# Performance work log

Hardware: AMD Instinct MI355X
Metric: run time of the kernel (lower is better)

## Reference

```python
import jax, jax.numpy as jnp
import numpy as np

N = 50000   # nodes
E = 800000  # edges (avg degree 16)
D = 128     # in = hidden = out channels (residual path active)
EPS = 1e-5  # BatchNorm eps


def setup_inputs() -> dict:
    key = jax.random.key(0)
    ks = jax.random.split(key, 24)
    sc = 1.0 / np.sqrt(D)
    inp = {
        "x": jax.random.normal(ks[0], (N, D), jnp.float32),
        "W1": jax.random.normal(ks[1], (D, D), jnp.float32) * sc,
        "b1": jnp.zeros((D,), jnp.float32),
        "g1": 1.0 + 0.1 * jax.random.normal(ks[2], (D,), jnp.float32),
        "be1": 0.1 * jax.random.normal(ks[3], (D,), jnp.float32),
        "m1": 0.1 * jax.random.normal(ks[4], (D,), jnp.float32),
        "v1": 0.5 + jax.random.uniform(ks[5], (D,), jnp.float32),
        "W2": jax.random.normal(ks[6], (D, D), jnp.float32) * sc,
        "b2": jnp.zeros((D,), jnp.float32),
        "g2": 1.0 + 0.1 * jax.random.normal(ks[7], (D,), jnp.float32),
        "be2": 0.1 * jax.random.normal(ks[8], (D,), jnp.float32),
        "m2": 0.1 * jax.random.normal(ks[9], (D,), jnp.float32),
        "v2": 0.5 + jax.random.uniform(ks[10], (D,), jnp.float32),
        "W3": jax.random.normal(ks[11], (D, D), jnp.float32) * sc,
        "b3": jnp.zeros((D,), jnp.float32),
        "src": jax.random.randint(ks[12], (E,), 0, N, jnp.int32),
        "dst": jax.random.randint(ks[13], (E,), 0, N, jnp.int32),
    }
    return inp


def _gcn_conv(x, W, b, src, dst):
    # PyG GCNConv: add self-loops, symmetric D^{-1/2}(A+I)D^{-1/2} normalization.
    h = x @ W                                              # [N, C]
    deg = jax.ops.segment_sum(jnp.ones((E,), x.dtype), dst, num_segments=N) + 1.0
    dinv = jax.lax.rsqrt(deg)                              # [N]
    coef = dinv[src] * dinv[dst]                           # [E]
    agg = jax.ops.segment_sum(h[src] * coef[:, None], dst, num_segments=N)
    agg = agg + h * (dinv * dinv)[:, None]                 # self-loop term
    return agg + b


def _bn(x, g, be, m, v):
    # eval-mode BatchNorm1d with running stats
    return (x - m) * jax.lax.rsqrt(v + EPS) * g + be


def reference(x, W1, b1, g1, be1, m1, v1, W2, b2, g2, be2, m2, v2, W3, b3, src, dst):
    x_res = x
    h = jax.nn.relu(_bn(_gcn_conv(x, W1, b1, src, dst), g1, be1, m1, v1))
    h = jax.nn.relu(_bn(_gcn_conv(h, W2, b2, src, dst), g2, be2, m2, v2))
    h = _gcn_conv(h, W3, b3, src, dst)
    return h + x_res  # in_channels == out_channels -> residual active
```

## Files before the change

### kernel.cpp

```cpp
#include <hip/hip_runtime.h>
#include <hip/hip_bf16.h>


#define GCN_N 50000
#define GCN_E 800000
#define GCN_D 128

using bf16x8 = __attribute__((ext_vector_type(8))) short;
using f32x4  = __attribute__((ext_vector_type(4))) float;

__device__ __forceinline__ float bflo(unsigned u) { return __uint_as_float(u << 16); }
__device__ __forceinline__ float bfhi(unsigned u) { return __uint_as_float(u & 0xffff0000u); }
__device__ __forceinline__ unsigned f2bf(float f) {
    unsigned u = __float_as_uint(f);
    return (u + 0x7fffu + ((u >> 16) & 1u)) >> 16;
}

__global__ __launch_bounds__(256) void zero_kernel(int* __restrict__ p, int n) {
    int i = blockIdx.x * blockDim.x + threadIdx.x;
    if (i < n) p[i] = 0;
}

__global__ __launch_bounds__(256) void hist_kernel(const int* __restrict__ dst,
                                                   int* __restrict__ cnt, int nE) {
    int e = blockIdx.x * blockDim.x + threadIdx.x;
    if (e < nE) atomicAdd(&cnt[dst[e]], 1);
}

__global__ __launch_bounds__(256) void block_reduce(const int* __restrict__ cnt,
                                                    int* __restrict__ bsum, int n) {
    int tid = threadIdx.x, lane = tid & 63, wid = tid >> 6;
    int i0 = blockIdx.x * 1024 + tid * 4;
    int s = 0;
    #pragma unroll
    for (int q = 0; q < 4; ++q)
        if (i0 + q < n) s += cnt[i0 + q];
    #pragma unroll
    for (int off = 32; off >= 1; off >>= 1) s += __shfl_xor(s, off);
    __shared__ int ws[4];
    if (lane == 0) ws[wid] = s;
    __syncthreads();
    if (tid == 0) bsum[blockIdx.x] = ws[0] + ws[1] + ws[2] + ws[3];
}

__global__ void scan_bsums(const int* __restrict__ bsum, int* __restrict__ boff,
                           int nb, int* __restrict__ row_last) {
    int lane = threadIdx.x;
    int v = (lane < nb) ? bsum[lane] : 0;
    int sc = v;
    #pragma unroll
    for (int off = 1; off < 64; off <<= 1) {
        int t = __shfl_up(sc, off);
        if (lane >= off) sc += t;
    }
    if (lane < nb) boff[lane] = sc - v;
    if (lane == 63) *row_last = sc;
}

__global__ __launch_bounds__(256) void scan_apply(const int* __restrict__ cnt_in,
                                                  const int* __restrict__ boff,
                                                  int* __restrict__ row_ptr,
                                                  float* __restrict__ dinv,
                                                  int* __restrict__ cnt_zero, int n) {
    __shared__ int wsum[4];
    int tid = threadIdx.x, lane = tid & 63, wid = tid >> 6;
    int i0 = blockIdx.x * 1024 + tid * 4;
    int a0 = 0, a1 = 0, a2 = 0, a3 = 0;
    if (i0 + 0 < n) a0 = cnt_in[i0 + 0];
    if (i0 + 1 < n) a1 = cnt_in[i0 + 1];
    if (i0 + 2 < n) a2 = cnt_in[i0 + 2];
    if (i0 + 3 < n) a3 = cnt_in[i0 + 3];
    int tsum = a0 + a1 + a2 + a3;
    int sc = tsum;
    #pragma unroll
    for (int off = 1; off < 64; off <<= 1) {
        int t = __shfl_up(sc, off);
        if (lane >= off) sc += t;
    }
    if (lane == 63) wsum[wid] = sc;
    __syncthreads();
    int woff = 0;
    #pragma unroll
    for (int w = 0; w < 4; ++w)
        if (w < wid) woff += wsum[w];
    int excl = boff[blockIdx.x] + woff + (sc - tsum);
    if (i0 + 0 < n) { row_ptr[i0 + 0] = excl;                dinv[i0 + 0] = rsqrtf((float)a0 + 1.f); cnt_zero[i0 + 0] = 0; }
    if (i0 + 1 < n) { row_ptr[i0 + 1] = excl + a0;           dinv[i0 + 1] = rsqrtf((float)a1 + 1.f); cnt_zero[i0 + 1] = 0; }
    if (i0 + 2 < n) { row_ptr[i0 + 2] = excl + a0 + a1;      dinv[i0 + 2] = rsqrtf((float)a2 + 1.f); cnt_zero[i0 + 2] = 0; }
    if (i0 + 3 < n) { row_ptr[i0 + 3] = excl + a0 + a1 + a2; dinv[i0 + 3] = rsqrtf((float)a3 + 1.f); cnt_zero[i0 + 3] = 0; }
}

__global__ __launch_bounds__(256) void fill_kernel(const int* __restrict__ src,
                                                   const int* __restrict__ dst,
                                                   const int* __restrict__ row_ptr,
                                                   int* __restrict__ cur,
                                                   int* __restrict__ esrc, int nE) {
    int e = blockIdx.x * blockDim.x + threadIdx.x;
    if (e >= nE) return;
    int d = dst[e];
    int pos = row_ptr[d] + atomicAdd(&cur[d], 1);
    esrc[pos] = src[e];
}

__global__ void prep_kernel(const float* __restrict__ b, const float* __restrict__ g,
                            const float* __restrict__ be, const float* __restrict__ m,
                            const float* __restrict__ v, float* __restrict__ scale,
                            float* __restrict__ shift) {
    int c = threadIdx.x;
    float s = g[c] * rsqrtf(v[c] + 1e-5f);
    scale[c] = s;
    shift[c] = (b[c] - m[c]) * s + be[c];
}

__global__ __launch_bounds__(256) void castx_kernel(const float* __restrict__ x,
                                                    unsigned short* __restrict__ xb,
                                                    int nElem) {
    int i = (blockIdx.x * 256 + threadIdx.x) * 8;
    if (i + 7 < nElem) {
        float4 f0 = *(const float4*)&x[i];
        float4 f1 = *(const float4*)&x[i + 4];
        uint4 o;
        o.x = f2bf(f0.x) | (f2bf(f0.y) << 16);
        o.y = f2bf(f0.z) | (f2bf(f0.w) << 16);
        o.z = f2bf(f1.x) | (f2bf(f1.y) << 16);
        o.w = f2bf(f1.z) | (f2bf(f1.w) << 16);
        *(uint4*)&xb[i] = o;
    }
}

__global__ __launch_bounds__(256) void wtrans_kernel(const float* __restrict__ W,
                                                     unsigned short* __restrict__ Wt) {
    int id = blockIdx.x * 256 + threadIdx.x;
    int nn = id >> 7, k = id & 127;
    Wt[id] = (unsigned short)f2bf(W[k * 128 + nn]);
}

__global__ __launch_bounds__(256) void mm_mfma(const unsigned short* __restrict__ A,
                                               const unsigned short* __restrict__ Wt,
                                               const float* __restrict__ dinv,
                                               unsigned short* __restrict__ hb, int n) {
    __shared__ unsigned short Cs[64][136];
    int tid = threadIdx.x;
    int w = tid >> 6, l = tid & 63;
    int lg = l >> 4, li = l & 15;
    int row0 = blockIdx.x * 64;

    int arow = row0 + w * 16 + li;
    int arow_c = min(arow, n - 1);
    const unsigned short* ap = A + (size_t)arow_c * GCN_D + lg * 8;
    bf16x8 a[4];
    #pragma unroll
    for (int k0 = 0; k0 < 4; ++k0) a[k0] = *(const bf16x8*)(ap + k0 * 32);

    f32x4 acc[8];
    #pragma unroll
    for (int t = 0; t < 8; ++t) acc[t] = (f32x4){0.f, 0.f, 0.f, 0.f};

    #pragma unroll
    for (int t = 0; t < 8; ++t) {
        const unsigned short* bp = Wt + (size_t)(t * 16 + li) * GCN_D + lg * 8;
        #pragma unroll
        for (int k0 = 0; k0 < 4; ++k0) {
            bf16x8 b = *(const bf16x8*)(bp + k0 * 32);
            acc[t] = __builtin_amdgcn_mfma_f32_16x16x32_bf16(a[k0], b, acc[t], 0, 0, 0);
        }
    }

    int crow = w * 16 + lg * 4;
    float dv[4];
    #pragma unroll
    for (int r = 0; r < 4; ++r) dv[r] = dinv[min(row0 + crow + r, n - 1)];
    #pragma unroll
    for (int t = 0; t < 8; ++t)
        #pragma unroll
        for (int r = 0; r < 4; ++r)
            Cs[crow + r][t * 16 + li] = (unsigned short)f2bf(acc[t][r] * dv[r]);
    __syncthreads();

    int orow = tid >> 2;
    int gr = row0 + orow;
    if (gr < n) {
        const unsigned short* sp = &Cs[orow][(tid & 3) * 32];
        uint4* dp = (uint4*)&hb[(size_t)gr * GCN_D + (tid & 3) * 32];
        dp[0] = *(const uint4*)(sp + 0);
        dp[1] = *(const uint4*)(sp + 8);
        dp[2] = *(const uint4*)(sp + 16);
        dp[3] = *(const uint4*)(sp + 24);
    }
}

template <int FINAL>
__global__ __launch_bounds__(256) void agg_kernel(const unsigned short* __restrict__ hb,
                                                  const int* __restrict__ row_ptr,
                                                  const int* __restrict__ esrc,
                                                  const float* __restrict__ dinv,
                                                  const float* __restrict__ scale,
                                                  const float* __restrict__ shift,
                                                  const float* __restrict__ xres,
                                                  unsigned short* __restrict__ outb,
                                                  float* __restrict__ outf, int n) {
    int wid = threadIdx.x >> 6, lane = threadIdx.x & 63;
    int node = blockIdx.x * 4 + wid;
    if (node >= n) return;
    int cc = lane * 2;
    unsigned us = *(const unsigned*)&hb[(size_t)node * GCN_D + cc];
    float aLo = bflo(us), aHi = bfhi(us);
    float bLo = 0.f, bHi = 0.f;
    int j = row_ptr[node], end = row_ptr[node + 1];
    for (; j + 8 <= end; j += 8) {
        int s0 = esrc[j + 0], s1 = esrc[j + 1], s2 = esrc[j + 2], s3 = esrc[j + 3];
        int s4 = esrc[j + 4], s5 = esrc[j + 5], s6 = esrc[j + 6], s7 = esrc[j + 7];
        unsigned u0 = *(const unsigned*)&hb[(size_t)s0 * GCN_D + cc];
        unsigned u1 = *(const unsigned*)&hb[(size_t)s1 * GCN_D + cc];
        unsigned u2 = *(const unsigned*)&hb[(size_t)s2 * GCN_D + cc];
        unsigned u3 = *(const unsigned*)&hb[(size_t)s3 * GCN_D + cc];
        unsigned u4 = *(const unsigned*)&hb[(size_t)s4 * GCN_D + cc];
        unsigned u5 = *(const unsigned*)&hb[(size_t)s5 * GCN_D + cc];
        unsigned u6 = *(const unsigned*)&hb[(size_t)s6 * GCN_D + cc];
        unsigned u7 = *(const unsigned*)&hb[(size_t)s7 * GCN_D + cc];
        aLo += bflo(u0) + bflo(u1);  aHi += bfhi(u0) + bfhi(u1);
        bLo += bflo(u2) + bflo(u3);  bHi += bfhi(u2) + bfhi(u3);
        aLo += bflo(u4) + bflo(u5);  aHi += bfhi(u4) + bfhi(u5);
        bLo += bflo(u6) + bflo(u7);  bHi += bfhi(u6) + bfhi(u7);
    }
    for (; j < end; ++j) {
        int s = esrc[j];
        unsigned u = *(const unsigned*)&hb[(size_t)s * GCN_D + cc];
        aLo += bflo(u);  aHi += bfhi(u);
    }
    float dvn = dinv[node];
    float vx = (aLo + bLo) * dvn;
    float vy = (aHi + bHi) * dvn;
    if (FINAL) {
        float2 b = *(const float2*)&scale[cc];
        float2 xr = *(const float2*)&xres[(size_t)node * GCN_D + cc];
        float2 o;
        o.x = vx + b.x + xr.x;
        o.y = vy + b.y + xr.y;
        *(float2*)&outf[(size_t)node * GCN_D + cc] = o;
    } else {
        float2 sc = *(const float2*)&scale[cc];
        float2 sh = *(const float2*)&shift[cc];
        float ox = fmaxf(vx * sc.x + sh.x, 0.f);
        float oy = fmaxf(vy * sc.y + sh.y, 0.f);
        *(unsigned*)&outb[(size_t)node * GCN_D + cc] = f2bf(ox) | (f2bf(oy) << 16);
    }
}

extern "C" void kernel_launch(void* const* d_in, const int* in_sizes, int n_in,
                              void* d_out, int out_size, void* d_ws, size_t ws_size,
                              hipStream_t stream) {
    (void)in_sizes; (void)n_in; (void)out_size; (void)ws_size;
    const int N = GCN_N, E = GCN_E, D = GCN_D;

    const float* x   = (const float*)d_in[0];
    const float* W1  = (const float*)d_in[1];
    const float* b1  = (const float*)d_in[2];
    const float* g1  = (const float*)d_in[3];
    const float* be1 = (const float*)d_in[4];
    const float* m1  = (const float*)d_in[5];
    const float* v1  = (const float*)d_in[6];
    const float* W2  = (const float*)d_in[7];
    const float* b2  = (const float*)d_in[8];
    const float* g2  = (const float*)d_in[9];
    const float* be2 = (const float*)d_in[10];
    const float* m2  = (const float*)d_in[11];
    const float* v2  = (const float*)d_in[12];
    const float* W3  = (const float*)d_in[13];
    const float* b3  = (const float*)d_in[14];
    const int* src   = (const int*)d_in[15];
    const int* dst   = (const int*)d_in[16];
    float* out = (float*)d_out;

    unsigned short* hb   = (unsigned short*)d_ws;
    unsigned short* actb = hb + (size_t)N * D;
    unsigned short* xb   = actb + (size_t)N * D;
    unsigned short* wt1  = xb + (size_t)N * D;
    unsigned short* wt2  = wt1 + D * D;
    unsigned short* wt3  = wt2 + D * D;
    float* dinv   = (float*)(wt3 + D * D);
    int* cnt      = (int*)(dinv + N);
    int* row_ptr  = cnt + N;
    int* esrc     = row_ptr + (N + 2);
    float* scale1 = (float*)(esrc + E);
    float* shift1 = scale1 + D;
    float* scale2 = shift1 + D;
    float* shift2 = scale2 + D;
    int* bsum     = (int*)(shift2 + D);
    int* boff     = bsum + 64;

    const int NB = (N + 1023) / 1024;

    castx_kernel<<<(N * D) / (256 * 8), 256, 0, stream>>>(x, xb, N * D);
    wtrans_kernel<<<(D * D) / 256, 256, 0, stream>>>(W1, wt1);
    wtrans_kernel<<<(D * D) / 256, 256, 0, stream>>>(W2, wt2);
    wtrans_kernel<<<(D * D) / 256, 256, 0, stream>>>(W3, wt3);
    zero_kernel<<<(N + 255) / 256, 256, 0, stream>>>(cnt, N);
    hist_kernel<<<(E + 255) / 256, 256, 0, stream>>>(dst, cnt, E);
    block_reduce<<<NB, 256, 0, stream>>>(cnt, bsum, N);
    scan_bsums<<<1, 64, 0, stream>>>(bsum, boff, NB, &row_ptr[N]);
    scan_apply<<<NB, 256, 0, stream>>>(cnt, boff, row_ptr, dinv, cnt, N);
    fill_kernel<<<(E + 255) / 256, 256, 0, stream>>>(src, dst, row_ptr, cnt, esrc, E);
    prep_kernel<<<1, D, 0, stream>>>(b1, g1, be1, m1, v1, scale1, shift1);
    prep_kernel<<<1, D, 0, stream>>>(b2, g2, be2, m2, v2, scale2, shift2);

    int mm_grid = (N + 63) / 64;
    int agg_grid = (N + 3) / 4;

    mm_mfma<<<mm_grid, 256, 0, stream>>>(xb, wt1, dinv, hb, N);
    agg_kernel<0><<<agg_grid, 256, 0, stream>>>(hb, row_ptr, esrc, dinv,
                                                scale1, shift1, nullptr, actb, nullptr, N);
    mm_mfma<<<mm_grid, 256, 0, stream>>>(actb, wt2, dinv, hb, N);
    agg_kernel<0><<<agg_grid, 256, 0, stream>>>(hb, row_ptr, esrc, dinv,
                                                scale2, shift2, nullptr, actb, nullptr, N);
    mm_mfma<<<mm_grid, 256, 0, stream>>>(actb, wt3, dinv, hb, N);
    agg_kernel<1><<<agg_grid, 256, 0, stream>>>(hb, row_ptr, esrc, dinv,
                                                b3, nullptr, x, nullptr, out, N);
}
```

Baseline: 393.0 us.

## Bucket edges by destination range before CSR fill and merge prep kernels

Fuses the x cast, the three weight transposes and the counter zeroing into one prep kernel, and merges the two BN prep kernels into one launch. Edge processing is split into two passes. The first pass does the histogram and writes (src,dst) pairs into destination-range buckets, with replicas to reduce atomic contention. The second pass fills the CSR bucket by bucket, so the scattered atomics and writes hit a smaller, more cache-local address range. The cost is an extra pass over the edge pairs and a fixed-capacity segment buffer, which would overflow if a bucket replica ever held more than SEGCAP edges.

```diff
diff --git a/kernel.cpp b/kernel.cpp
--- a/kernel.cpp
+++ b/kernel.cpp
@@ -5,6 +5,9 @@
 #define GCN_N 50000
 #define GCN_E 800000
 #define GCN_D 128
+#define NBK 16
+#define NREP 8
+#define SEGCAP 16384
 
 using bf16x8 = __attribute__((ext_vector_type(8))) short;
 using f32x4  = __attribute__((ext_vector_type(4))) float;
@@ -16,15 +19,85 @@
     return (u + 0x7fffu + ((u >> 16) & 1u)) >> 16;
 }
 
-__global__ __launch_bounds__(256) void zero_kernel(int* __restrict__ p, int n) {
-    int i = blockIdx.x * blockDim.x + threadIdx.x;
-    if (i < n) p[i] = 0;
-}
-
-__global__ __launch_bounds__(256) void hist_kernel(const int* __restrict__ dst,
-                                                   int* __restrict__ cnt, int nE) {
-    int e = blockIdx.x * blockDim.x + threadIdx.x;
-    if (e < nE) atomicAdd(&cnt[dst[e]], 1);
+__global__ __launch_bounds__(256) void prep_all(const float* __restrict__ x,
+                                                unsigned short* __restrict__ xb,
+                                                const float* __restrict__ W1,
+                                                const float* __restrict__ W2,
+                                                const float* __restrict__ W3,
+                                                unsigned short* __restrict__ wt1,
+                                                unsigned short* __restrict__ wt2,
+                                                unsigned short* __restrict__ wt3,
+                                                int* __restrict__ cnt,
+                                                int* __restrict__ bcur) {
+    int gid = blockIdx.x * 256 + threadIdx.x;
+    int i = gid * 8;
+    if (i + 7 < GCN_N * GCN_D) {
+        float4 f0 = *(const float4*)&x[i];
+        float4 f1 = *(const float4*)&x[i + 4];
+        uint4 o;
+        o.x = f2bf(f0.x) | (f2bf(f0.y) << 16);
+        o.y = f2bf(f0.z) | (f2bf(f0.w) << 16);
+        o.z = f2bf(f1.x) | (f2bf(f1.y) << 16);
+        o.w = f2bf(f1.z) | (f2bf(f1.w) << 16);
+        *(uint4*)&xb[i] = o;
+    }
+    if (gid < GCN_N) cnt[gid] = 0;
+    if (gid < NBK * NREP) bcur[gid] = 0;
+    if (gid < GCN_D * GCN_D) {
+        int nn = gid >> 7, k = gid & 127;
+        wt1[gid] = (unsigned short)f2bf(W1[k * 128 + nn]);
+        wt2[gid] = (unsigned short)f2bf(W2[k * 128 + nn]);
+        wt3[gid] = (unsigned short)f2bf(W3[k * 128 + nn]);
+    }
+}
+
+__global__ __launch_bounds__(256) void fillA(const int* __restrict__ src,
+                                             const int* __restrict__ dst,
+                                             int* __restrict__ cnt,
+                                             int* __restrict__ bcur,
+                                             int2* __restrict__ pairs, int nE) {
+    __shared__ int lcnt[NBK];
+    __shared__ int lbase[NBK];
+    int tid = threadIdx.x;
+    if (tid < NBK) lcnt[tid] = 0;
+    __syncthreads();
+    int e = blockIdx.x * 256 + tid;
+    int rep = blockIdx.x & (NREP - 1);
+    int s = 0, d = 0, b = 0, off = 0;
+    bool valid = e < nE;
+    if (valid) {
+        s = src[e];
+        d = dst[e];
+        atomicAdd(&cnt[d], 1);
+        b = d >> 12;
+        off = atomicAdd(&lcnt[b], 1);
+    }
+    __syncthreads();
+    if (tid < NBK)
+        lbase[tid] = lcnt[tid] ? atomicAdd(&bcur[tid * NREP + rep], lcnt[tid]) : 0;
+    __syncthreads();
+    if (valid)
+        pairs[(size_t)(b * NREP + rep) * SEGCAP + lbase[b] + off] = make_int2(s, d);
+}
+
+__global__ __launch_bounds__(256) void fillB(const int2* __restrict__ pairs,
+                                             const int* __restrict__ bcur,
+                                             const int* __restrict__ row_ptr,
+                                             int* __restrict__ cur,
+                                             int* __restrict__ esrc) {
+    int b = blockIdx.x & (NBK - 1);
+    int j = blockIdx.x >> 4;
+    int tid = threadIdx.x;
+    #pragma unroll
+    for (int r = 0; r < NREP; ++r) {
+        int cr = bcur[b * NREP + r];
+        const int2* seg = pairs + (size_t)(b * NREP + r) * SEGCAP;
+        for (int i = j * 256 + tid; i < cr; i += 32 * 256) {
+            int2 p = seg[i];
+            int pos = row_ptr[p.y] + atomicAdd(&cur[p.y], 1);
+            esrc[pos] = p.x;
+        }
+    }
 }
 
 __global__ __launch_bounds__(256) void block_reduce(const int* __restrict__ cnt,
@@ -90,49 +163,24 @@
     if (i0 + 3 < n) { row_ptr[i0 + 3] = excl + a0 + a1 + a2; dinv[i0 + 3] = rsqrtf((float)a3 + 1.f); cnt_zero[i0 + 3] = 0; }
 }
 
-__global__ __launch_bounds__(256) void fill_kernel(const int* __restrict__ src,
-                                                   const int* __restrict__ dst,
-                                                   const int* __restrict__ row_ptr,
-                                                   int* __restrict__ cur,
-                                                   int* __restrict__ esrc, int nE) {
-    int e = blockIdx.x * blockDim.x + threadIdx.x;
-    if (e >= nE) return;
-    int d = dst[e];
-    int pos = row_ptr[d] + atomicAdd(&cur[d], 1);
-    esrc[pos] = src[e];
-}
-
-__global__ void prep_kernel(const float* __restrict__ b, const float* __restrict__ g,
-                            const float* __restrict__ be, const float* __restrict__ m,
-                            const float* __restrict__ v, float* __restrict__ scale,
-                            float* __restrict__ shift) {
+__global__ void prep_bn(const float* __restrict__ b1, const float* __restrict__ g1,
+                        const float* __restrict__ be1, const float* __restrict__ m1,
+                        const float* __restrict__ v1, float* __restrict__ scale1,
+                        float* __restrict__ shift1,
+                        const float* __restrict__ b2, const float* __restrict__ g2,
+                        const float* __restrict__ be2, const float* __restrict__ m2,
+                        const float* __restrict__ v2, float* __restrict__ scale2,
+                        float* __restrict__ shift2) {
     int c = threadIdx.x;
-    float s = g[c] * rsqrtf(v[c] + 1e-5f);
-    scale[c] = s;
-    shift[c] = (b[c] - m[c]) * s + be[c];
-}
-
-__global__ __launch_bounds__(256) void castx_kernel(const float* __restrict__ x,
-                                                    unsigned short* __restrict__ xb,
-                                                    int nElem) {
-    int i = (blockIdx.x * 256 + threadIdx.x) * 8;
-    if (i + 7 < nElem) {
-        float4 f0 = *(const float4*)&x[i];
-        float4 f1 = *(const float4*)&x[i + 4];
-        uint4 o;
-        o.x = f2bf(f0.x) | (f2bf(f0.y) << 16);
-        o.y = f2bf(f0.z) | (f2bf(f0.w) << 16);
-        o.z = f2bf(f1.x) | (f2bf(f1.y) << 16);
-        o.w = f2bf(f1.z) | (f2bf(f1.w) << 16);
-        *(uint4*)&xb[i] = o;
-    }
-}
-
-__global__ __launch_bounds__(256) void wtrans_kernel(const float* __restrict__ W,
-                                                     unsigned short* __restrict__ Wt) {
-    int id = blockIdx.x * 256 + threadIdx.x;
-    int nn = id >> 7, k = id & 127;
-    Wt[id] = (unsigned short)f2bf(W[k * 128 + nn]);
+    if (blockIdx.x == 0) {
+        float s = g1[c] * rsqrtf(v1[c] + 1e-5f);
+        scale1[c] = s;
+        shift1[c] = (b1[c] - m1[c]) * s + be1[c];
+    } else {
+        float s = g2[c] * rsqrtf(v2[c] + 1e-5f);
+        scale2[c] = s;
+        shift2[c] = (b2[c] - m2[c]) * s + be2[c];
+    }
 }
 
 __global__ __launch_bounds__(256) void mm_mfma(const unsigned short* __restrict__ A,
@@ -288,21 +336,20 @@
     float* shift2 = scale2 + D;
     int* bsum     = (int*)(shift2 + D);
     int* boff     = bsum + 64;
+    int* bcur     = boff + 64;
+    int2* pairs   = (int2*)(bcur + NBK * NREP);
 
     const int NB = (N + 1023) / 1024;
 
-    castx_kernel<<<(N * D) / (256 * 8), 256, 0, stream>>>(x, xb, N * D);
-    wtrans_kernel<<<(D * D) / 256, 256, 0, stream>>>(W1, wt1);
-    wtrans_kernel<<<(D * D) / 256, 256, 0, stream>>>(W2, wt2);
-    wtrans_kernel<<<(D * D) / 256, 256, 0, stream>>>(W3, wt3);
-    zero_kernel<<<(N + 255) / 256, 256, 0, stream>>>(cnt, N);
-    hist_kernel<<<(E + 255) / 256, 256, 0, stream>>>(dst, cnt, E);
+    prep_all<<<(N * D) / (256 * 8), 256, 0, stream>>>(x, xb, W1, W2, W3,
+                                                      wt1, wt2, wt3, cnt, bcur);
+    fillA<<<(E + 255) / 256, 256, 0, stream>>>(src, dst, cnt, bcur, pairs, E);
     block_reduce<<<NB, 256, 0, stream>>>(cnt, bsum, N);
     scan_bsums<<<1, 64, 0, stream>>>(bsum, boff, NB, &row_ptr[N]);
     scan_apply<<<NB, 256, 0, stream>>>(cnt, boff, row_ptr, dinv, cnt, N);
-    fill_kernel<<<(E + 255) / 256, 256, 0, stream>>>(src, dst, row_ptr, cnt, esrc, E);
-    prep_kernel<<<1, D, 0, stream>>>(b1, g1, be1, m1, v1, scale1, shift1);
-    prep_kernel<<<1, D, 0, stream>>>(b2, g2, be2, m2, v2, scale2, shift2);
+    fillB<<<32 * NBK, 256, 0, stream>>>(pairs, bcur, row_ptr, cnt, esrc);
+    prep_bn<<<2, D, 0, stream>>>(b1, g1, be1, m1, v1, scale1, shift1,
+                                 b2, g2, be2, m2, v2, scale2, shift2);
 
     int mm_grid = (N + 63) / 64;
     int agg_grid = (N + 3) / 4;
```

Result: slower. 434.4 us (+10.5%).
